# Performance work log

Hardware: AMD Instinct MI355X
Metric: run time of the kernel (lower is better)

The kernel has to match this reference:

```python
import jax, jax.numpy as jnp
import numpy as np

VOCAB = 2548
EMBED = 1000


def setup_inputs() -> dict:
    key = jax.random.key(0)
    kx, kw = jax.random.split(key)
    x = jax.random.randint(kx, (64, 512), 0, VOCAB, dtype=jnp.int64 if jax.config.jax_enable_x64 else jnp.int32)
    # torch kaiming_uniform_(a=sqrt(5)) on [V, E]: fan_in = E, bound = 1/sqrt(fan_in)
    bound = 1.0 / np.sqrt(EMBED)
    weight = jax.random.uniform(kw, (VOCAB, EMBED), minval=-bound, maxval=bound, dtype=jnp.float32)
    return {"x": x, "weight": weight}


def reference(x, weight):
    # Faithful to the original: build one-hot rows from an identity matrix
    # (self.mat[x]) and do a dense matmul against the embedding weight.
    onehot = jax.nn.one_hot(x, VOCAB, dtype=weight.dtype)        # [B, S, V]
    emb = jnp.einsum('bsv,ve->bse', onehot, weight)              # [B, S, E]
    return emb.reshape(x.shape[0], -1)                           # [B, S*E]
```

## Files before the change

### kernel.cpp

```cpp
#include <hip/hip_runtime.h>


constexpr int VOCAB          = 2548;
constexpr int CHUNKS_PER_ROW = 250;
constexpr int ROWS           = 64 * 512;
constexpr int TOTAL_CHUNKS   = ROWS * CHUNKS_PER_ROW;
constexpr int BLOCKS         = 2000;
constexpr int THREADS        = 256;
constexpr int NTHR           = BLOCKS * THREADS;
constexpr int K              = TOTAL_CHUNKS / NTHR;

typedef unsigned int u32x4 __attribute__((ext_vector_type(4)));

__global__ __launch_bounds__(THREADS)
void embed_gather_f32_kernel(const int* __restrict__ x,
                             const u32x4* __restrict__ w,
                             u32x4* __restrict__ out)
{
    const int c0 = blockIdx.x * THREADS + threadIdx.x;

    #pragma unroll
    for (int b = 0; b < K / 4; ++b) {
        int off[4], idx[4];
        u32x4 v[4];
        #pragma unroll
        for (int j = 0; j < 4; ++j) {
            const int c   = c0 + (b * 4 + j) * NTHR;
            const int row = c / CHUNKS_PER_ROW;
            off[j] = c - row * CHUNKS_PER_ROW;
            idx[j] = min(max(x[row], 0), VOCAB - 1);
        }
        #pragma unroll
        for (int j = 0; j < 4; ++j)
            v[j] = w[idx[j] * CHUNKS_PER_ROW + off[j]];
        #pragma unroll
        for (int j = 0; j < 4; ++j)
            __builtin_nontemporal_store(v[j], &out[c0 + (b * 4 + j) * NTHR]);
    }
}

extern "C" void kernel_launch(void* const* d_in, const int* in_sizes, int n_in,
                              void* d_out, int out_size, void* d_ws, size_t ws_size,
                              hipStream_t stream) {
    int xi = 0, wi = 0;
    for (int i = 1; i < n_in; ++i) {
        if (in_sizes[i] < in_sizes[xi]) xi = i;
        if (in_sizes[i] > in_sizes[wi]) wi = i;
    }
    if (xi == wi && n_in >= 2) { xi = 0; wi = 1; }

    const int*   x = (const int*)d_in[xi];
    const u32x4* w = (const u32x4*)d_in[wi];
    u32x4*       o = (u32x4*)d_out;

    embed_gather_f32_kernel<<<BLOCKS, THREADS, 0, stream>>>(x, w, o);
}
```

Measured before the change: 38.18 us.

## Replace per-chunk gather with per-vocab-row scatter using shared-memory index queues

Each block now loads two embedding rows into registers once, scans the full index array in segments, builds shared-memory queues of matching positions with atomics, and writes the row to each matching output location. This removes the repeated random reads of weight rows and the per-chunk index division. In exchange, every block rereads the whole index tensor and adds barriers per segment. Out-of-range indices are no longer clamped and are simply never written.

```diff
diff --git a/kernel.cpp b/kernel.cpp
--- a/kernel.cpp
+++ b/kernel.cpp
@@ -1,41 +1,66 @@
 #include <hip/hip_runtime.h>
 
 
-constexpr int VOCAB          = 2548;
-constexpr int CHUNKS_PER_ROW = 250;
-constexpr int ROWS           = 64 * 512;
-constexpr int TOTAL_CHUNKS   = ROWS * CHUNKS_PER_ROW;
-constexpr int BLOCKS         = 2000;
-constexpr int THREADS        = 256;
-constexpr int NTHR           = BLOCKS * THREADS;
-constexpr int K              = TOTAL_CHUNKS / NTHR;
+constexpr int VOCAB   = 2548;
+constexpr int ECHUNK  = 250;
+constexpr int ROWS    = 64 * 512;
+constexpr int VPB     = 2;
+constexpr int GRID    = VOCAB / VPB;
+constexpr int THREADS = 256;
+constexpr int SEG     = 2048;
+constexpr int NSEG    = ROWS / SEG;
 
 typedef unsigned int u32x4 __attribute__((ext_vector_type(4)));
 
 __global__ __launch_bounds__(THREADS)
-void embed_gather_f32_kernel(const int* __restrict__ x,
-                             const u32x4* __restrict__ w,
-                             u32x4* __restrict__ out)
+void embed_scatter_kernel(const int* __restrict__ x,
+                          const u32x4* __restrict__ w,
+                          u32x4* __restrict__ out)
 {
-    const int c0 = blockIdx.x * THREADS + threadIdx.x;
+    __shared__ int q[VPB][SEG];
+    __shared__ int qcnt[VPB];
+    const int v0 = blockIdx.x * VPB;
+    const int t  = threadIdx.x;
 
-    #pragma unroll
-    for (int b = 0; b < K / 4; ++b) {
-        int off[4], idx[4];
-        u32x4 v[4];
+    u32x4 row[VPB];
+    if (t < ECHUNK) {
         #pragma unroll
-        for (int j = 0; j < 4; ++j) {
-            const int c   = c0 + (b * 4 + j) * NTHR;
-            const int row = c / CHUNKS_PER_ROW;
-            off[j] = c - row * CHUNKS_PER_ROW;
-            idx[j] = min(max(x[row], 0), VOCAB - 1);
+        for (int k = 0; k < VPB; ++k) row[k] = w[(v0 + k) * ECHUNK + t];
+    }
+
+    const int4* x4 = (const int4*)x;
+
+    for (int s = 0; s < NSEG; ++s) {
+        if (t < VPB) qcnt[t] = 0;
+        __syncthreads();
+
+        #pragma unroll
+        for (int u = 0; u < SEG / 4 / THREADS; ++u) {
+            const int i4   = s * (SEG / 4) + u * THREADS + t;
+            const int4 xv  = x4[i4];
+            const int base = i4 * 4;
+            const int e[4] = { xv.x, xv.y, xv.z, xv.w };
+            #pragma unroll
+            for (int j = 0; j < 4; ++j) {
+                const unsigned d = (unsigned)(e[j] - v0);
+                if (d < (unsigned)VPB) {
+                    const int slot = atomicAdd(&qcnt[d], 1);
+                    q[d][slot] = base + j;
+                }
+            }
         }
+        __syncthreads();
+
         #pragma unroll
-        for (int j = 0; j < 4; ++j)
-            v[j] = w[idx[j] * CHUNKS_PER_ROW + off[j]];
-        #pragma unroll
-        for (int j = 0; j < 4; ++j)
-            __builtin_nontemporal_store(v[j], &out[c0 + (b * 4 + j) * NTHR]);
+        for (int k = 0; k < VPB; ++k) {
+            const int n = qcnt[k];
+            for (int j = 0; j < n; ++j) {
+                const int p = q[k][j];
+                if (t < ECHUNK)
+                    __builtin_nontemporal_store(row[k], &out[p * ECHUNK + t]);
+            }
+        }
+        __syncthreads();
     }
 }
 
@@ -53,5 +78,5 @@
     const u32x4* w = (const u32x4*)d_in[wi];
     u32x4*       o = (u32x4*)d_out;
 
-    embed_gather_f32_kernel<<<BLOCKS, THREADS, 0, stream>>>(x, w, o);
+    embed_scatter_kernel<<<GRID, THREADS, 0, stream>>>(x, w, o);
 }
```

Result: faster. 35.21 us, median of 2 (-7.8%).
